# Optimization experiments

Measured on AMD Instinct MI355X. Metric: run time of the kernel, lower is better.

The kernel has to match this reference:

```python
import jax, jax.numpy as jnp
import numpy as np

L = 3          # num_layer
EMB = 128      # emb_dim
NODE_F = 32    # node_feat_dim
EDGE_F = 16    # edge_feat_dim
TASKS = 1
N_GRAPHS = 64
EPS = 1e-5     # BatchNorm eps


def setup_inputs() -> dict:
    key = jax.random.key(0)
    ks = jax.random.split(key, 16)
    N, E = 50000, 800000
    x = jax.random.normal(ks[0], (N, NODE_F), dtype=jnp.float32)
    edge_index = jax.random.randint(ks[1], (2, E), 0, N, dtype=jnp.int32)
    edge_attr = jax.random.normal(ks[2], (E, EDGE_F), dtype=jnp.float32)
    batch = jnp.sort(jax.random.randint(ks[3], (N,), 0, N_GRAPHS, dtype=jnp.int32))
    s = lambda *sh: 1.0 / np.sqrt(sh[-1])
    # input node embedding
    W0 = jax.random.normal(ks[4], (EMB, NODE_F), dtype=jnp.float32) * s(EMB, NODE_F)
    b0 = jnp.zeros((EMB,), jnp.float32)
    # per-layer params, stacked over L
    We = jax.random.normal(ks[5], (L, EMB, EDGE_F), dtype=jnp.float32) * s(EMB, EDGE_F)
    be = jnp.zeros((L, EMB), jnp.float32)
    W1 = jax.random.normal(ks[6], (L, 2 * EMB, EMB), dtype=jnp.float32) * s(2 * EMB, EMB)
    b1 = jnp.zeros((L, 2 * EMB), jnp.float32)
    W2 = jax.random.normal(ks[7], (L, EMB, 2 * EMB), dtype=jnp.float32) * s(EMB, 2 * EMB)
    b2 = jnp.zeros((L, EMB), jnp.float32)
    gamma = jnp.ones((L, EMB), jnp.float32)
    beta = jnp.zeros((L, EMB), jnp.float32)
    # graph prediction head
    Wp = jax.random.normal(ks[8], (TASKS, EMB), dtype=jnp.float32) * s(TASKS, EMB)
    bp = jnp.zeros((TASKS,), jnp.float32)
    return {"x": x, "edge_attr": edge_attr, "W0": W0, "b0": b0, "We": We, "be": be,
            "W1": W1, "b1": b1, "W2": W2, "b2": b2, "gamma": gamma, "beta": beta,
            "Wp": Wp, "bp": bp, "edge_index": edge_index, "batch": batch}


def _forward(x, edge_attr, W0, b0, We, be, W1, b1, W2, b2, gamma, beta, Wp, bp,
             edge_index, batch):
    N = x.shape[0]
    src, dst = edge_index[0], edge_index[1]
    self_idx = jnp.arange(N, dtype=src.dtype)
    src_full = jnp.concatenate([src, self_idx])  # [E+N] with self loops
    dst_full = jnp.concatenate([dst, self_idx])
    h = x @ W0.T + b0  # [N, EMB]
    for l in range(L):
        # edge embedding; self-loop edge_attr is zeros -> embedding is just bias
        e_emb = edge_attr @ We[l].T + be[l]                       # [E, EMB]
        e_self = jnp.broadcast_to(be[l], (N, EMB))                # [N, EMB]
        msgs = h[src_full] + jnp.concatenate([e_emb, e_self], 0)  # [E+N, EMB]
        aggr = jax.ops.segment_sum(msgs, dst_full, num_segments=N)
        h2 = jax.nn.relu(aggr @ W1[l].T + b1[l]) @ W2[l].T + b2[l]
        # BatchNorm1d (training-mode batch statistics, biased var)
        mu = jnp.mean(h2, axis=0)
        var = jnp.mean(jnp.square(h2 - mu), axis=0)
        h = gamma[l] * (h2 - mu) * jax.lax.rsqrt(var + EPS) + beta[l]
        if l < L - 1:
            h = jax.nn.relu(h)
    # global mean pool over graphs
    sums = jax.ops.segment_sum(h, batch, num_segments=N_GRAPHS)
    cnts = jax.ops.segment_sum(jnp.ones((N,), h.dtype), batch, num_segments=N_GRAPHS)
    pooled = sums / jnp.maximum(cnts, 1.0)[:, None]
    return pooled @ Wp.T + bp  # [N_GRAPHS, TASKS]


def reference(x, edge_attr, W0, b0, We, be, W1, b1, W2, b2, gamma, beta, Wp, bp,
              edge_index, batch):
    return _forward(x, edge_attr, W0, b0, We, be, W1, b1, W2, b2, gamma, beta,
                    Wp, bp, edge_index, batch)
```

## Files before the change

### kernel.cpp

```cpp
#include <hip/hip_runtime.h>
#include <stdint.h>

#define EMB 128
#define LAYERS 3
#define NGRAPHS 64
#define BN_EPS 1e-5f

#define BSH 6
#define BNODES 64
#define SUBCAP 256
#define BCAP (8 * SUBCAP + 256)
#define OVFCAP 8192

typedef short short8 __attribute__((ext_vector_type(8)));
typedef float float4v __attribute__((ext_vector_type(4)));
typedef unsigned short ushort4v __attribute__((ext_vector_type(4)));

__device__ __forceinline__ unsigned short f2bf(float f) {
    union { float f; unsigned int i; } v; v.f = f;
    unsigned int x = v.i;
    unsigned int r = x + 0x7FFFu + ((x >> 16) & 1u);
    return (unsigned short)(r >> 16);
}
__device__ __forceinline__ float bflo(unsigned int u) {
    union { unsigned int i; float f; } v; v.i = u << 16; return v.f;
}
__device__ __forceinline__ float bfhi(unsigned int u) {
    union { unsigned int i; float f; } v; v.i = u & 0xffff0000u; return v.f;
}
__device__ __forceinline__ unsigned int packbf(float a, float b) {
    return (unsigned int)f2bf(a) | ((unsigned int)f2bf(b) << 16);
}

__global__ __launch_bounds__(256) void conv_bf16_3(
    const float* __restrict__ a, unsigned short* __restrict__ oa, int na,
    const float* __restrict__ b, unsigned short* __restrict__ ob, int nb,
    const float* __restrict__ c, unsigned short* __restrict__ oc, int nc)
{
    int i = blockIdx.x * 256 + threadIdx.x;
    int stride = gridDim.x * 256;
    for (int t = i; t < na + nb + nc; t += stride) {
        if (t < na) oa[t] = f2bf(a[t]);
        else if (t < na + nb) ob[t - na] = f2bf(b[t - na]);
        else oc[t - na - nb] = f2bf(c[t - na - nb]);
    }
}

template<int K, bool A_IS_BF16, bool RELU, bool OUT_BF16>
__global__ __launch_bounds__(256) void gemm_bt(
    const void* __restrict__ Av, const unsigned short* __restrict__ B,
    const float* __restrict__ bias, void* __restrict__ Cv,
    int M, int Ntot)
{
    const int wave = threadIdx.x >> 6;
    const int lane = threadIdx.x & 63;
    const int q    = lane >> 4;
    const int ln   = lane & 15;
    const int m_base = blockIdx.x * 64 + wave * 16;
    const int n_base = blockIdx.y * 64;

    float4v acc[4];
#pragma unroll
    for (int i = 0; i < 4; ++i) acc[i] = (float4v){0.f, 0.f, 0.f, 0.f};

    int mrow = m_base + ln;
    if (mrow >= M) mrow = M - 1;

    const int KSTEPS = K / 32;
#pragma unroll
    for (int ks = 0; ks < KSTEPS; ++ks) {
        const int k0 = ks * 32 + q * 8;
        short8 afrag;
        if constexpr (A_IS_BF16) {
            const unsigned short* A = (const unsigned short*)Av;
            afrag = *reinterpret_cast<const short8*>(A + (size_t)mrow * K + k0);
        } else {
            const float* A = (const float*)Av;
            const float4v* p = reinterpret_cast<const float4v*>(A + (size_t)mrow * K + k0);
            float4v f0 = p[0], f1 = p[1];
            afrag[0] = (short)f2bf(f0[0]); afrag[1] = (short)f2bf(f0[1]);
            afrag[2] = (short)f2bf(f0[2]); afrag[3] = (short)f2bf(f0[3]);
            afrag[4] = (short)f2bf(f1[0]); afrag[5] = (short)f2bf(f1[1]);
            afrag[6] = (short)f2bf(f1[2]); afrag[7] = (short)f2bf(f1[3]);
        }
#pragma unroll
        for (int nt = 0; nt < 4; ++nt) {
            const short8 bfrag = *reinterpret_cast<const short8*>(
                B + (size_t)(n_base + nt * 16 + ln) * K + k0);
            acc[nt] = __builtin_amdgcn_mfma_f32_16x16x32_bf16(afrag, bfrag, acc[nt], 0, 0, 0);
        }
    }

#pragma unroll
    for (int nt = 0; nt < 4; ++nt) {
        const int n = n_base + nt * 16 + ln;
        const float bv = bias[n];
#pragma unroll
        for (int r = 0; r < 4; ++r) {
            const int m = m_base + q * 4 + r;
            if (m < M) {
                float v = acc[nt][r] + bv;
                if constexpr (RELU) v = v > 0.f ? v : 0.f;
                if constexpr (OUT_BF16)
                    ((unsigned short*)Cv)[(size_t)m * Ntot + n] = f2bf(v);
                else
                    ((float*)Cv)[(size_t)m * Ntot + n] = v;
            }
        }
    }
}

__global__ __launch_bounds__(512) void fused_mlp(
    const unsigned short* __restrict__ ag, const unsigned short* __restrict__ W1,
    const float* __restrict__ b1, const unsigned short* __restrict__ W2,
    const float* __restrict__ b2, float* __restrict__ h2,
    float* __restrict__ sums2, int M, int ntiles)
{
    __shared__ unsigned short ag_lds[32 * 136];
    __shared__ unsigned short Ylds[32 * 264];
    const int tid = threadIdx.x;
    const int wave = tid >> 6, lane = tid & 63;
    const int q = lane >> 4, ln = lane & 15;
    const int k0 = q * 8;
    float* slice = sums2 + (size_t)(blockIdx.x & 31) * 256;

    short8 w1f[2][4], w2f[8];
#pragma unroll
    for (int c = 0; c < 2; ++c) {
        const int ct = wave * 2 + c;
#pragma unroll
        for (int ks = 0; ks < 4; ++ks)
            w1f[c][ks] = *reinterpret_cast<const short8*>(
                W1 + (size_t)(ct * 16 + ln) * 128 + ks * 32 + k0);
    }
#pragma unroll
    for (int ks = 0; ks < 8; ++ks)
        w2f[ks] = *reinterpret_cast<const short8*>(
            W2 + (size_t)(wave * 16 + ln) * 256 + ks * 32 + k0);
    float4v b1v[2];
    b1v[0] = *reinterpret_cast<const float4v*>(b1 + (wave * 2) * 16 + q * 4);
    b1v[1] = *reinterpret_cast<const float4v*>(b1 + (wave * 2 + 1) * 16 + q * 4);
    const float4v b2v = *reinterpret_cast<const float4v*>(b2 + wave * 16 + q * 4);

    for (int t = blockIdx.x; t < ntiles; t += gridDim.x) {
        const int nbase = t * 32;
        __syncthreads();
        {
            const int nd = tid >> 4, ch = (tid & 15) * 8;
            int ng = nbase + nd; if (ng >= M) ng = M - 1;
            *reinterpret_cast<uint4*>(&ag_lds[nd * 136 + ch]) =
                *reinterpret_cast<const uint4*>(ag + (size_t)ng * 128 + ch);
        }
        __syncthreads();

#pragma unroll
        for (int nt = 0; nt < 2; ++nt) {
            short8 agf[4];
#pragma unroll
            for (int ks = 0; ks < 4; ++ks)
                agf[ks] = *reinterpret_cast<const short8*>(
                    &ag_lds[(nt * 16 + ln) * 136 + ks * 32 + k0]);
#pragma unroll
            for (int c = 0; c < 2; ++c) {
                float4v acc = (float4v){0.f, 0.f, 0.f, 0.f};
#pragma unroll
                for (int ks = 0; ks < 4; ++ks)
                    acc = __builtin_amdgcn_mfma_f32_16x16x32_bf16(
                        w1f[c][ks], agf[ks], acc, 0, 0, 0);
                const int c0 = (wave * 2 + c) * 16 + q * 4;
                ushort4v pk;
                pk[0] = f2bf(fmaxf(acc[0] + b1v[c][0], 0.f));
                pk[1] = f2bf(fmaxf(acc[1] + b1v[c][1], 0.f));
                pk[2] = f2bf(fmaxf(acc[2] + b1v[c][2], 0.f));
                pk[3] = f2bf(fmaxf(acc[3] + b1v[c][3], 0.f));
                *reinterpret_cast<ushort4v*>(&Ylds[(nt * 16 + ln) * 264 + c0]) = pk;
            }
        }
        __syncthreads();

        float s[4], s2[4];
#pragma unroll
        for (int r = 0; r < 4; ++r) { s[r] = 0.f; s2[r] = 0.f; }
        const int c0 = wave * 16 + q * 4;
#pragma unroll
        for (int nt = 0; nt < 2; ++nt) {
            short8 yf[8];
#pragma unroll
            for (int ks = 0; ks < 8; ++ks)
                yf[ks] = *reinterpret_cast<const short8*>(
                    &Ylds[(nt * 16 + ln) * 264 + ks * 32 + k0]);
            float4v acc = (float4v){0.f, 0.f, 0.f, 0.f};
#pragma unroll
            for (int ks = 0; ks < 8; ++ks)
                acc = __builtin_amdgcn_mfma_f32_16x16x32_bf16(
                    w2f[ks], yf[ks], acc, 0, 0, 0);
            const int node = nbase + nt * 16 + ln;
            const bool valid = (node < M);
            float4v v;
            v[0] = acc[0] + b2v[0]; v[1] = acc[1] + b2v[1];
            v[2] = acc[2] + b2v[2]; v[3] = acc[3] + b2v[3];
            if (valid)
                *reinterpret_cast<float4v*>(h2 + (size_t)node * 128 + c0) = v;
#pragma unroll
            for (int r = 0; r < 4; ++r) {
                const float x = valid ? v[r] : 0.f;
                s[r] += x; s2[r] += x * x;
            }
        }
#pragma unroll
        for (int off = 1; off < 16; off <<= 1) {
#pragma unroll
            for (int r = 0; r < 4; ++r) {
                s[r]  += __shfl_xor(s[r],  off);
                s2[r] += __shfl_xor(s2[r], off);
            }
        }
        if (ln == 0) {
#pragma unroll
            for (int r = 0; r < 4; ++r) {
                atomicAdd(&slice[c0 + r], s[r]);
                atomicAdd(&slice[128 + c0 + r], s2[r]);
            }
        }
    }
}

__global__ __launch_bounds__(128) void bn_coef(
    const float* __restrict__ sums2, const float* __restrict__ gamma,
    const float* __restrict__ beta, float* __restrict__ coef, float invN)
{
    const int c = threadIdx.x;
    float s = 0.f, ss = 0.f;
    for (int k = 0; k < 32; ++k) {
        s  += sums2[k * 256 + c];
        ss += sums2[k * 256 + 128 + c];
    }
    float mu = s * invN;
    float var = ss * invN - mu * mu;
    float sc = gamma[c] * rsqrtf(fmaxf(var, 0.f) + BN_EPS);
    coef[c] = sc;
    coef[128 + c] = beta[c] - mu * sc;
}

__global__ __launch_bounds__(256) void edge_scatter(
    const int* __restrict__ ei, int* __restrict__ subcnt,
    uint2* __restrict__ staging, int* __restrict__ ovfcnt,
    uint4* __restrict__ ovfbuf, int E)
{
    const int sub = blockIdx.x & 7;
    const int e = blockIdx.x * 256 + threadIdx.x;
    if (e >= E) return;
    const unsigned int src = (unsigned int)ei[e];
    const int dst = ei[E + e];
    const int b = dst >> BSH;
    const unsigned int rx = src | ((unsigned int)(dst & (BNODES - 1)) << 16);
    const int sl = b * 8 + sub;
    const int pos = atomicAdd(&subcnt[sl], 1);
    if (pos < SUBCAP) {
        staging[(size_t)sl * SUBCAP + pos] = make_uint2(rx, (unsigned int)e);
    } else {
        int op = atomicAdd(ovfcnt, 1);
        if (op < OVFCAP)
            ovfbuf[op] = make_uint4(rx, (unsigned int)e, (unsigned int)b, 0u);
    }
}

__global__ __launch_bounds__(256) void bucket_scan(
    const int* __restrict__ subcnt, int* __restrict__ bucketbase, int B)
{
    const int t = threadIdx.x;
    int tot[4]; int mysum = 0;
#pragma unroll
    for (int j = 0; j < 4; ++j) {
        const int b = t * 4 + j;
        int s = 0;
        if (b < B)
            for (int k = 0; k < 8; ++k) s += subcnt[b * 8 + k];
        tot[j] = s; mysum += s;
    }
    const int lane = t & 63, wv = t >> 6;
    int iv = mysum;
#pragma unroll
    for (int off = 1; off < 64; off <<= 1) {
        int u = __shfl_up(iv, off);
        if (lane >= off) iv += u;
    }
    __shared__ int ws[4];
    if (lane == 63) ws[wv] = iv;
    __syncthreads();
    int woff = 0;
    for (int j = 0; j < wv; ++j) woff += ws[j];
    int ex = woff + iv - mysum;
#pragma unroll
    for (int j = 0; j < 4; ++j) {
        const int b = t * 4 + j;
        if (b < B) bucketbase[b] = ex;
        ex += tot[j];
    }
    if (t == 255) bucketbase[B] = ex;
}

__global__ __launch_bounds__(256) void csr_build(
    const int* __restrict__ subcnt, const int* __restrict__ bucketbase,
    const uint2* __restrict__ staging, const int* __restrict__ ovfcnt,
    const uint4* __restrict__ ovfbuf,
    int2* __restrict__ adj, int* __restrict__ rowptr, int N, int E)
{
    __shared__ uint2 recs[BCAP];
    __shared__ int scnt[8], sp[8], cnt[BNODES], rp_s[BNODES], wp2[BNODES];
    __shared__ int totsh;
    const int b = blockIdx.x;
    const int tid = threadIdx.x;
    if (tid < 8) scnt[tid] = min(subcnt[b * 8 + tid], SUBCAP);
    if (tid < BNODES) cnt[tid] = 0;
    __syncthreads();
    if (tid == 0) {
        int a = 0;
        for (int s = 0; s < 8; ++s) { sp[s] = a; a += scnt[s]; }
        totsh = a;
    }
    __syncthreads();
    for (int s = 0; s < 8; ++s) {
        const int L = scnt[s];
        const uint2* srcp = staging + (size_t)(b * 8 + s) * SUBCAP;
        for (int i = tid; i < L; i += 256) {
            uint2 r = srcp[i];
            recs[sp[s] + i] = r;
            atomicAdd(&cnt[(r.x >> 16) & (BNODES - 1)], 1);
        }
    }
    __syncthreads();
    const int ov = min(*ovfcnt, OVFCAP);
    if (ov > 0) {
        for (int i = tid; i < ov; i += 256) {
            uint4 r = ovfbuf[i];
            if ((int)r.z == b) {
                int p = atomicAdd(&totsh, 1);
                if (p < BCAP) {
                    recs[p] = make_uint2(r.x, r.y);
                    atomicAdd(&cnt[(r.x >> 16) & (BNODES - 1)], 1);
                }
            }
        }
    }
    __syncthreads();
    const int total = min(totsh, BCAP);
    if (tid < BNODES) {
        int v = cnt[tid];
        int iv = v;
#pragma unroll
        for (int off = 1; off < 64; off <<= 1) {
            int u = __shfl_up(iv, off);
            if (tid >= off) iv += u;
        }
        rp_s[tid] = iv - v;
        wp2[tid] = 0;
    }
    __syncthreads();
    const int base = bucketbase[b];
    const int n0 = b * BNODES;
    const int nn = min(BNODES, N - n0);
    if (tid < nn) rowptr[n0 + tid] = base + rp_s[tid];
    if (b == 0 && tid == 0) rowptr[N] = E;
    for (int i = tid; i < total; i += 256) {
        uint2 r = recs[i];
        const int d = (r.x >> 16) & (BNODES - 1);
        const int pos = rp_s[d] + atomicAdd(&wp2[d], 1);
        adj[base + pos] = make_int2((int)(r.x & 0xFFFFu), (int)r.y);
    }
}

__global__ __launch_bounds__(256) void mom_gather(
    const int2* __restrict__ adj, const int* __restrict__ rowptr,
    const float* __restrict__ eattr, float* __restrict__ mom, int N)
{
    const int lane = threadIdx.x & 63;
    const int gwave = (blockIdx.x * 256 + threadIdx.x) >> 6;
    const int nwaves = (gridDim.x * 256) >> 6;
    const int j = lane >> 4, k = lane & 15;
    for (int n = gwave; n < N; n += nwaves) {
        const int s = rowptr[n], e = rowptr[n + 1];
        float acc = 0.f;
        for (int p = s + j; p < e; p += 4) {
            const int eid = adj[p].y;
            acc += eattr[(size_t)eid * 16 + k];
        }
        acc += __shfl_xor(acc, 16);
        acc += __shfl_xor(acc, 32);
        if (lane < 16) mom[(size_t)n * 16 + lane] = acc;
    }
}

__global__ __launch_bounds__(256) void aggregate_kernel(
    const unsigned short* __restrict__ h, const int2* __restrict__ adj,
    const int* __restrict__ rowptr, const float* __restrict__ mom,
    const float* __restrict__ We, const float* __restrict__ be,
    unsigned short* __restrict__ ag, int N)
{
    const int lane = threadIdx.x & 63;
    const int gwave = (blockIdx.x * 256 + threadIdx.x) >> 6;
    const int nwaves = (gridDim.x * 256) >> 6;
    const int c0 = 2 * lane;

    float w0[16], w1[16];
#pragma unroll
    for (int k = 0; k < 16; ++k) {
        w0[k] = We[c0 * 16 + k];
        w1[k] = We[(c0 + 1) * 16 + k];
    }
    const float b0 = be[c0], b1 = be[c0 + 1];

    for (int n = gwave; n < N; n += nwaves) {
        const int s = rowptr[n], e = rowptr[n + 1];
        unsigned int self = *reinterpret_cast<const unsigned int*>(
            h + (size_t)n * 128 + c0);
        float ax = bflo(self), ay = bfhi(self);
        float mval = (lane < 16) ? mom[(size_t)n * 16 + lane] : 0.f;

        int p = s;
        for (; p + 16 <= e; p += 16) {
            int idx[16];
#pragma unroll
            for (int j = 0; j < 16; ++j) idx[j] = adj[p + j].x;
            unsigned int vv[16];
#pragma unroll
            for (int j = 0; j < 16; ++j)
                vv[j] = *reinterpret_cast<const unsigned int*>(
                    h + (size_t)idx[j] * 128 + c0);
#pragma unroll
            for (int j = 0; j < 16; ++j) { ax += bflo(vv[j]); ay += bfhi(vv[j]); }
        }
        for (; p < e; p += 8) {
            int idx[8];
#pragma unroll
            for (int j = 0; j < 8; ++j) {
                const int pp = p + j;
                idx[j] = (pp < e) ? adj[pp].x : N;
            }
            unsigned int vv[8];
#pragma unroll
            for (int j = 0; j < 8; ++j)
                vv[j] = *reinterpret_cast<const unsigned int*>(
                    h + (size_t)idx[j] * 128 + c0);
#pragma unroll
            for (int j = 0; j < 8; ++j) { ax += bflo(vv[j]); ay += bfhi(vv[j]); }
        }

        const float degp1 = (float)(e - s + 1);
        float d0 = b0 * degp1, d1 = b1 * degp1;
#pragma unroll
        for (int k = 0; k < 16; ++k) {
            const float sk = __shfl(mval, k);
            d0 += w0[k] * sk; d1 += w1[k] * sk;
        }
        ax += d0; ay += d1;
        *reinterpret_cast<unsigned int*>(ag + (size_t)n * 128 + c0) = packbf(ax, ay);
    }
}

__global__ __launch_bounds__(256) void bn_apply_bf16(
    const float* __restrict__ h2, const float* __restrict__ coef,
    unsigned short* __restrict__ h, int total4)
{
    int tid = blockIdx.x * 256 + threadIdx.x;
    int c4 = (tid * 4) & 127;
    float sc[4], sh[4];
#pragma unroll
    for (int j = 0; j < 4; ++j) {
        sc[j] = coef[c4 + j];
        sh[j] = coef[128 + c4 + j];
    }
    int stride = gridDim.x * 256;
    for (int i = tid; i < total4; i += stride) {
        float4v v = reinterpret_cast<const float4v*>(h2)[i];
        float x0 = fmaxf(sc[0] * v[0] + sh[0], 0.f);
        float x1 = fmaxf(sc[1] * v[1] + sh[1], 0.f);
        float x2 = fmaxf(sc[2] * v[2] + sh[2], 0.f);
        float x3 = fmaxf(sc[3] * v[3] + sh[3], 0.f);
        uint2 o; o.x = packbf(x0, x1); o.y = packbf(x2, x3);
        reinterpret_cast<uint2*>(h)[i] = o;
    }
}

__global__ __launch_bounds__(256) void pool_part(
    const float* __restrict__ h2, const int* __restrict__ batch,
    float* __restrict__ pooled, int N)
{
    const int per = (N + gridDim.x - 1) / gridDim.x;
    const int start = blockIdx.x * per;
    const int end = min(start + per, N);
    if (start >= end) return;
    const int c = threadIdx.x & 127;
    const int sub = threadIdx.x >> 7;
    int g_cur = batch[start];
    float acc = 0.f;
    for (int n = start + sub; n < end; n += 2) {
        int g = batch[n];
        if (g != g_cur) {
            if (acc != 0.f) atomicAdd(&pooled[(size_t)g_cur * 128 + c], acc);
            acc = 0.f; g_cur = g;
        }
        acc += h2[(size_t)n * 128 + c];
    }
    if (acc != 0.f) atomicAdd(&pooled[(size_t)g_cur * 128 + c], acc);
}

__global__ __launch_bounds__(128) void head_final(
    const float* __restrict__ pooled, const int* __restrict__ batch,
    const float* __restrict__ coef, const float* __restrict__ Wp,
    const float* __restrict__ bp, float* __restrict__ out, int N)
{
    const int g = blockIdx.x;
    __shared__ int sb[2];
    if (threadIdx.x < 2) {
        int target = g + threadIdx.x;
        int lo = 0, hi = N;
        while (lo < hi) {
            int mid = (lo + hi) >> 1;
            if (batch[mid] < target) lo = mid + 1; else hi = mid;
        }
        sb[threadIdx.x] = lo;
    }
    __syncthreads();
    const float cntf = fmaxf((float)(sb[1] - sb[0]), 1.f);
    const int c = threadIdx.x;
    float m = pooled[(size_t)g * 128 + c] / cntf;
    float v = (coef[c] * m + coef[128 + c]) * Wp[c];
    const int lane = threadIdx.x & 63;
#pragma unroll
    for (int off = 32; off > 0; off >>= 1) v += __shfl_down(v, off);
    __shared__ float wsum[2];
    if (lane == 0) wsum[threadIdx.x >> 6] = v;
    __syncthreads();
    if (threadIdx.x == 0) out[g] = wsum[0] + wsum[1] + bp[0];
}

extern "C" void kernel_launch(void* const* d_in, const int* in_sizes, int n_in,
                              void* d_out, int out_size, void* d_ws, size_t ws_size,
                              hipStream_t stream)
{
    const float* x     = (const float*)d_in[0];
    const float* eattr = (const float*)d_in[1];
    const float* W0    = (const float*)d_in[2];
    const float* b0    = (const float*)d_in[3];
    const float* We    = (const float*)d_in[4];
    const float* be    = (const float*)d_in[5];
    const float* W1    = (const float*)d_in[6];
    const float* b1    = (const float*)d_in[7];
    const float* W2    = (const float*)d_in[8];
    const float* b2    = (const float*)d_in[9];
    const float* gamma = (const float*)d_in[10];
    const float* beta  = (const float*)d_in[11];
    const float* Wp    = (const float*)d_in[12];
    const float* bp    = (const float*)d_in[13];
    const int* ei    = (const int*)d_in[14];
    const int* batch = (const int*)d_in[15];

    const int N = in_sizes[0] / 32;
    const int E = in_sizes[1] / 16;
    const int NB = (N + BNODES - 1) / BNODES;

    char* ws = (char*)d_ws;
    size_t off = 0;
    auto alloc = [&](size_t bytes) { char* p = ws + off; off += (bytes + 255) & ~(size_t)255; return p; };
    unsigned short* hb = (unsigned short*)alloc((size_t)(N + 1) * 128 * 2);
    unsigned short* ag = (unsigned short*)alloc((size_t)N * 128 * 2);
    float* h2 = (float*)alloc((size_t)N * 128 * 4);
    uint2* staging = (uint2*)h2;
    float* sums2   = (float*)alloc(32 * 256 * 4);
    float* coef    = (float*)alloc(256 * 4);
    float* pooled  = (float*)alloc(NGRAPHS * 128 * 4);
    float* mom     = (float*)alloc((size_t)N * 16 * 4);
    unsigned short* W0bf = (unsigned short*)alloc(128 * 32 * 2);
    unsigned short* W1bf = (unsigned short*)alloc(3 * 256 * 128 * 2);
    unsigned short* W2bf = (unsigned short*)alloc(3 * 128 * 256 * 2);
    int* rowptr   = (int*)alloc(((size_t)N + 1) * 4);
    int* subcnt   = (int*)alloc(((size_t)NB * 8 + 1) * 4);
    int* ovfcnt   = subcnt + NB * 8;
    int* bucketbase = (int*)alloc(((size_t)NB + 1) * 4);
    uint4* ovfbuf = (uint4*)alloc((size_t)OVFCAP * 16);
    int2* adj     = (int2*)alloc((size_t)E * 8);

    const dim3 blk(256);
    const int mblocks = (N + 63) / 64;
    const int mtiles = (N + 31) / 32;
    const int fblocks = (mtiles + 2) / 3;
    const int total4 = N * 32;
    const int eblocks = (E + 255) / 256;
    const float invN = 1.0f / (float)N;

    hipMemsetAsync(subcnt, 0, ((size_t)NB * 8 + 1) * 4, stream);
    hipMemsetAsync(hb + (size_t)N * 128, 0, 128 * 2, stream);
    edge_scatter<<<dim3(eblocks), blk, 0, stream>>>(
        ei, subcnt, staging, ovfcnt, ovfbuf, E);
    bucket_scan<<<dim3(1), blk, 0, stream>>>(subcnt, bucketbase, NB);
    csr_build<<<dim3(NB), blk, 0, stream>>>(
        subcnt, bucketbase, staging, ovfcnt, ovfbuf, adj, rowptr, N, E);
    mom_gather<<<dim3(2048), blk, 0, stream>>>(adj, rowptr, eattr, mom, N);

    conv_bf16_3<<<dim3(384), blk, 0, stream>>>(
        W0, W0bf, 128 * 32, W1, W1bf, 3 * 256 * 128, W2, W2bf, 3 * 128 * 256);

    gemm_bt<32, false, false, true><<<dim3(mblocks, 2), blk, 0, stream>>>(
        x, W0bf, b0, (void*)hb, N, 128);

    for (int l = 0; l < LAYERS; ++l) {
        hipMemsetAsync(sums2, 0, 32 * 256 * 4, stream);
        aggregate_kernel<<<dim3(2048), blk, 0, stream>>>(
            hb, adj, rowptr, mom, We + l * 128 * 16, be + l * 128, ag, N);
        fused_mlp<<<dim3(fblocks), dim3(512), 0, stream>>>(
            ag, W1bf + l * 256 * 128, b1 + l * 256,
            W2bf + l * 128 * 256, b2 + l * 128, h2, sums2, N, mtiles);
        bn_coef<<<dim3(1), dim3(128), 0, stream>>>(
            sums2, gamma + l * 128, beta + l * 128, coef, invN);
        if (l < LAYERS - 1)
            bn_apply_bf16<<<dim3(1024), blk, 0, stream>>>(h2, coef, hb, total4);
    }

    hipMemsetAsync(pooled, 0, NGRAPHS * 128 * 4, stream);
    pool_part<<<dim3(784), blk, 0, stream>>>(h2, batch, pooled, N);
    head_final<<<dim3(NGRAPHS), dim3(128), 0, stream>>>(
        pooled, batch, coef, Wp, bp, (float*)d_out, N);
}
```

Baseline: 471.2 us.

## Split adjacency into SoA arrays, scalarize indices, prefetch MLP tiles

```diff
diff --git a/kernel.cpp b/kernel.cpp
--- a/kernel.cpp
+++ b/kernel.cpp
@@ -142,16 +142,24 @@
     b1v[1] = *reinterpret_cast<const float4v*>(b1 + (wave * 2 + 1) * 16 + q * 4);
     const float4v b2v = *reinterpret_cast<const float4v*>(b2 + wave * 16 + q * 4);
 
+    const int nd = tid >> 4, ch = (tid & 15) * 8;
+    uint4 stage;
+    {
+        int ng = blockIdx.x * 32 + nd; if (ng >= M) ng = M - 1;
+        stage = *reinterpret_cast<const uint4*>(ag + (size_t)ng * 128 + ch);
+    }
+
     for (int t = blockIdx.x; t < ntiles; t += gridDim.x) {
         const int nbase = t * 32;
         __syncthreads();
-        {
-            const int nd = tid >> 4, ch = (tid & 15) * 8;
-            int ng = nbase + nd; if (ng >= M) ng = M - 1;
-            *reinterpret_cast<uint4*>(&ag_lds[nd * 136 + ch]) =
-                *reinterpret_cast<const uint4*>(ag + (size_t)ng * 128 + ch);
-        }
+        *reinterpret_cast<uint4*>(&ag_lds[nd * 136 + ch]) = stage;
         __syncthreads();
+
+        const int tn = t + gridDim.x;
+        if (tn < ntiles) {
+            int ng = tn * 32 + nd; if (ng >= M) ng = M - 1;
+            stage = *reinterpret_cast<const uint4*>(ag + (size_t)ng * 128 + ch);
+        }
 
 #pragma unroll
         for (int nt = 0; nt < 2; ++nt) {
@@ -304,7 +312,8 @@
     const int* __restrict__ subcnt, const int* __restrict__ bucketbase,
     const uint2* __restrict__ staging, const int* __restrict__ ovfcnt,
     const uint4* __restrict__ ovfbuf,
-    int2* __restrict__ adj, int* __restrict__ rowptr, int N, int E)
+    int* __restrict__ asrc, int* __restrict__ aeid,
+    int* __restrict__ rowptr, int N, int E)
 {
     __shared__ uint2 recs[BCAP];
     __shared__ int scnt[8], sp[8], cnt[BNODES], rp_s[BNODES], wp2[BNODES];
@@ -365,13 +374,14 @@
     for (int i = tid; i < total; i += 256) {
         uint2 r = recs[i];
         const int d = (r.x >> 16) & (BNODES - 1);
-        const int pos = rp_s[d] + atomicAdd(&wp2[d], 1);
-        adj[base + pos] = make_int2((int)(r.x & 0xFFFFu), (int)r.y);
+        const int pos = base + rp_s[d] + atomicAdd(&wp2[d], 1);
+        asrc[pos] = (int)(r.x & 0xFFFFu);
+        aeid[pos] = (int)r.y;
     }
 }
 
 __global__ __launch_bounds__(256) void mom_gather(
-    const int2* __restrict__ adj, const int* __restrict__ rowptr,
+    const int* __restrict__ aeid, const int* __restrict__ rowptr,
     const float* __restrict__ eattr, float* __restrict__ mom, int N)
 {
     const int lane = threadIdx.x & 63;
@@ -379,12 +389,21 @@
     const int nwaves = (gridDim.x * 256) >> 6;
     const int j = lane >> 4, k = lane & 15;
     for (int n = gwave; n < N; n += nwaves) {
-        const int s = rowptr[n], e = rowptr[n + 1];
+        const int s = __builtin_amdgcn_readfirstlane(rowptr[n]);
+        const int e = __builtin_amdgcn_readfirstlane(rowptr[n + 1]);
         float acc = 0.f;
-        for (int p = s + j; p < e; p += 4) {
-            const int eid = adj[p].y;
-            acc += eattr[(size_t)eid * 16 + k];
-        }
+        int p = s + j;
+        for (; p + 12 < e; p += 16) {
+            const int e0 = aeid[p], e1 = aeid[p + 4];
+            const int e2 = aeid[p + 8], e3 = aeid[p + 12];
+            const float v0 = eattr[(size_t)e0 * 16 + k];
+            const float v1 = eattr[(size_t)e1 * 16 + k];
+            const float v2 = eattr[(size_t)e2 * 16 + k];
+            const float v3 = eattr[(size_t)e3 * 16 + k];
+            acc += (v0 + v1) + (v2 + v3);
+        }
+        for (; p < e; p += 4)
+            acc += eattr[(size_t)aeid[p] * 16 + k];
         acc += __shfl_xor(acc, 16);
         acc += __shfl_xor(acc, 32);
         if (lane < 16) mom[(size_t)n * 16 + lane] = acc;
@@ -392,7 +411,7 @@
 }
 
 __global__ __launch_bounds__(256) void aggregate_kernel(
-    const unsigned short* __restrict__ h, const int2* __restrict__ adj,
+    const unsigned short* __restrict__ h, const int* __restrict__ asrc,
     const int* __restrict__ rowptr, const float* __restrict__ mom,
     const float* __restrict__ We, const float* __restrict__ be,
     unsigned short* __restrict__ ag, int N)
@@ -411,7 +430,8 @@
     const float b0 = be[c0], b1 = be[c0 + 1];
 
     for (int n = gwave; n < N; n += nwaves) {
-        const int s = rowptr[n], e = rowptr[n + 1];
+        const int s = __builtin_amdgcn_readfirstlane(rowptr[n]);
+        const int e = __builtin_amdgcn_readfirstlane(rowptr[n + 1]);
         unsigned int self = *reinterpret_cast<const unsigned int*>(
             h + (size_t)n * 128 + c0);
         float ax = bflo(self), ay = bfhi(self);
@@ -421,7 +441,8 @@
         for (; p + 16 <= e; p += 16) {
             int idx[16];
 #pragma unroll
-            for (int j = 0; j < 16; ++j) idx[j] = adj[p + j].x;
+            for (int j = 0; j < 16; ++j)
+                idx[j] = __builtin_amdgcn_readfirstlane(asrc[p + j]);
             unsigned int vv[16];
 #pragma unroll
             for (int j = 0; j < 16; ++j)
@@ -430,20 +451,22 @@
 #pragma unroll
             for (int j = 0; j < 16; ++j) { ax += bflo(vv[j]); ay += bfhi(vv[j]); }
         }
-        for (; p < e; p += 8) {
-            int idx[8];
-#pragma unroll
-            for (int j = 0; j < 8; ++j) {
+        if (p < e) {
+            int idx[16];
+#pragma unroll
+            for (int j = 0; j < 16; ++j) {
                 const int pp = p + j;
-                idx[j] = (pp < e) ? adj[pp].x : N;
+                const int sv = __builtin_amdgcn_readfirstlane(
+                    asrc[pp < e ? pp : e - 1]);
+                idx[j] = (pp < e) ? sv : N;
             }
-            unsigned int vv[8];
-#pragma unroll
-            for (int j = 0; j < 8; ++j)
+            unsigned int vv[16];
+#pragma unroll
+            for (int j = 0; j < 16; ++j)
                 vv[j] = *reinterpret_cast<const unsigned int*>(
                     h + (size_t)idx[j] * 128 + c0);
 #pragma unroll
-            for (int j = 0; j < 8; ++j) { ax += bflo(vv[j]); ay += bfhi(vv[j]); }
+            for (int j = 0; j < 16; ++j) { ax += bflo(vv[j]); ay += bfhi(vv[j]); }
         }
 
         const float degp1 = (float)(e - s + 1);
@@ -579,7 +602,8 @@
     int* ovfcnt   = subcnt + NB * 8;
     int* bucketbase = (int*)alloc(((size_t)NB + 1) * 4);
     uint4* ovfbuf = (uint4*)alloc((size_t)OVFCAP * 16);
-    int2* adj     = (int2*)alloc((size_t)E * 8);
+    int* asrc     = (int*)alloc((size_t)E * 4);
+    int* aeid     = (int*)alloc((size_t)E * 4);
 
     const dim3 blk(256);
     const int mblocks = (N + 63) / 64;
@@ -595,8 +619,8 @@
         ei, subcnt, staging, ovfcnt, ovfbuf, E);
     bucket_scan<<<dim3(1), blk, 0, stream>>>(subcnt, bucketbase, NB);
     csr_build<<<dim3(NB), blk, 0, stream>>>(
-        subcnt, bucketbase, staging, ovfcnt, ovfbuf, adj, rowptr, N, E);
-    mom_gather<<<dim3(2048), blk, 0, stream>>>(adj, rowptr, eattr, mom, N);
+        subcnt, bucketbase, staging, ovfcnt, ovfbuf, asrc, aeid, rowptr, N, E);
+    mom_gather<<<dim3(2048), blk, 0, stream>>>(aeid, rowptr, eattr, mom, N);
 
     conv_bf16_3<<<dim3(384), blk, 0, stream>>>(
         W0, W0bf, 128 * 32, W1, W1bf, 3 * 256 * 128, W2, W2bf, 3 * 128 * 256);
@@ -607,7 +631,7 @@
     for (int l = 0; l < LAYERS; ++l) {
         hipMemsetAsync(sums2, 0, 32 * 256 * 4, stream);
         aggregate_kernel<<<dim3(2048), blk, 0, stream>>>(
-            hb, adj, rowptr, mom, We + l * 128 * 16, be + l * 128, ag, N);
+            hb, asrc, rowptr, mom, We + l * 128 * 16, be + l * 128, ag, N);
         fused_mlp<<<dim3(fblocks), dim3(512), 0, stream>>>(
             ag, W1bf + l * 256 * 128, b1 + l * 256,
             W2bf + l * 128 * 256, b2 + l * 128, h2, sums2, N, mtiles);
```

After: 479.3 us. No clear change (+1.7%).
